# Optimization experiments

Measured on AMD Instinct MI355X. Metric: run time of the kernel, lower is better.

The kernel has to match this reference:

```python
import jax, jax.numpy as jnp
import numpy as np

DILATIONS = [1, 2, 4, 8, 16, 32, 64, 128, 256, 1, 2, 4, 8, 16, 32, 64, 128, 256]
KSIZE = 3
CHAN = 16
NUM_SIG = 1       # num_channels in original
NUM_CTRL = 3      # control channels appended to signal
FRAME_SIZE = 2048
R = sum(d * (KSIZE - 1) for d in DILATIONS) + 1  # 2045
BATCH = 64
T = FRAME_SIZE + R - 1  # 4092


def causal_conv1d(x, w, b, dil):
    # x: [B,T,Cin], w: [K,Cin,Cout] (Keras layout), causal left pad dil*(K-1)
    pad = dil * (w.shape[0] - 1)
    y = jax.lax.conv_general_dilated(
        x, w, window_strides=(1,), padding=[(pad, 0)],
        rhs_dilation=(dil,), dimension_numbers=("NWC", "WIO", "NWC"))
    return y + b


def setup_inputs() -> dict:
    key = jax.random.key(0)
    ks = jax.random.split(key, 8)
    n_layers = len(DILATIONS)
    in0 = NUM_SIG + NUM_CTRL            # layer 0 sees 1 signal + 3 controls = 4
    in_rest = CHAN + NUM_CTRL           # layers 1.. see 16-ch signal + 3 controls = 19
    s = 0.1
    inp = {
        "input": jax.random.normal(ks[0], (BATCH, T, in0), dtype=jnp.float32),
        "conv_w0": jax.random.normal(ks[1], (KSIZE, in0, CHAN), dtype=jnp.float32) * s,
        "conv_w": jax.random.normal(ks[2], (n_layers - 1, KSIZE, in_rest, CHAN), dtype=jnp.float32) * s,
        "conv_b": jax.random.normal(ks[3], (n_layers, CHAN), dtype=jnp.float32) * s,
        "io_w": jax.random.normal(ks[4], (n_layers - 1, CHAN, CHAN), dtype=jnp.float32) * s,
        "io_b": jax.random.normal(ks[5], (n_layers - 1, CHAN), dtype=jnp.float32) * s,
        "mixer_w": jax.random.normal(ks[6], (n_layers * CHAN, NUM_SIG), dtype=jnp.float32) * s,
        "mixer_b": jax.random.normal(ks[7], (NUM_SIG,), dtype=jnp.float32) * s,
    }
    return inp


def reference(input, conv_w0, conv_w, conv_b, io_w, io_b, mixer_w, mixer_b):
    signal = input[:, :, :NUM_SIG]        # [B,T,1]
    controls = input[:, :, NUM_SIG:]      # [B,T,3]
    n_layers = len(DILATIONS)
    acc = []
    for i in range(n_layers):
        w = conv_w0 if i == 0 else conv_w[i - 1]
        h = jnp.concatenate([signal, controls], axis=2)
        h = causal_conv1d(h, w, conv_b[i], DILATIONS[i])
        h = jax.nn.relu(h)                # [B,T,16]
        acc.append(h)
        if i != n_layers - 1:
            # 1x1 conv residual mix + halved channel-sum skip of previous signal
            signal = (jnp.einsum("btc,co->bto", h, io_w[i]) + io_b[i]
                      + jnp.sum(signal, axis=2, keepdims=True) / 2)
    accumulator = jnp.concatenate(acc, axis=2)  # [B,T,288]
    mixed = jnp.einsum("btc,co->bto", accumulator, mixer_w) + mixer_b
    return mixed[:, -FRAME_SIZE:, :]
```

## Files before the change

### kernel.cpp

```cpp
#include <hip/hip_runtime.h>

#define TFULL 4092
#define NB    64
#define CH    16
#define OUT_T 2048
#define TOFF  2044
#define GNT   512

template<int L0, int NL, int TILE, int HALO, bool FIRSTG>
__global__ __launch_bounds__(GNT, 4) void group2_kernel(
    const float* __restrict__ input,
    const float* __restrict__ conv_w0,
    const float* __restrict__ conv_w,
    const float* __restrict__ conv_b,
    const float* __restrict__ io_w,
    const float* __restrict__ io_b,
    const float* __restrict__ mixer_w,
    const float* __restrict__ mixer_b,
    const float* __restrict__ sig_in,
    float* __restrict__ sig_out,
    float* __restrict__ out,
    int out_start)
{
    constexpr int NROWS = TILE + HALO;
    __shared__ float4 buf4[4][NROWS];
    float4* pl0 = buf4[0]; float4* pl1 = buf4[1];
    float4* pl2 = buf4[2]; float4* pl3 = buf4[3];

    const int b       = blockIdx.y;
    const int tid     = threadIdx.x;
    const int tile_lo = out_start + blockIdx.x * TILE;
    const int tile_hi = (tile_lo + TILE < TFULL) ? (tile_lo + TILE) : TFULL;
    const int buf_lo  = tile_lo - HALO;
    const int jmax    = tile_hi - buf_lo;
    const int j0      = NROWS - 1024 + tid;
    const int j1      = NROWS - 512 + tid;

    const float4* ib4 = (const float4*)(input + (size_t)b * TFULL * 4);

    if constexpr (!FIRSTG) {
        const float* sp = sig_in + (size_t)b * TFULL * CH;
        for (int j = tid; j < jmax; j += GNT) {
            const float4* row = (const float4*)(sp + (size_t)(buf_lo + j) * CH);
            pl0[j] = row[0]; pl1[j] = row[1]; pl2[j] = row[2]; pl3[j] = row[3];
        }
        __syncthreads();
    }

    float acc0 = 0.f, acc1 = 0.f;
    int lo_off = 0;
    for (int i = 0; i < NL; ++i) {
        const int g   = L0 + i;
        const int dil = 1 << (g % 9);
        lo_off += 2 * dil;
        const bool lastl = (i == NL - 1);
        const float* wb   = (FIRSTG && g == 0) ? conv_w0
                                               : conv_w + (size_t)(g - 1) * 3 * 19 * CH;
        const float* bias = conv_b  + (size_t)g * CH;
        const float* iw   = io_w    + (size_t)g * CH * CH;
        const float* ob   = io_b    + (size_t)g * CH;
        const float* mw   = mixer_w + (size_t)g * CH;

        const bool a0 = (j0 >= lo_off) && (j0 < jmax);
        const bool a1 = (j1 >= lo_off) && (j1 < jmax);

        float sn0[CH], sn1[CH];

        auto row_compute = [&](int j, float* sn, float& accr) {
            float h[CH];
            #pragma unroll
            for (int o = 0; o < CH; ++o) h[o] = bias[o];
            float sum;
            if (FIRSTG && g == 0) {
                const float4 x0 = ib4[buf_lo + j - 2];
                const float4 x1 = ib4[buf_lo + j - 1];
                const float4 x2 = ib4[buf_lo + j];
                const float t0[4] = {x0.x, x0.y, x0.z, x0.w};
                const float t1[4] = {x1.x, x1.y, x1.z, x1.w};
                const float t2[4] = {x2.x, x2.y, x2.z, x2.w};
                #pragma unroll
                for (int cc = 0; cc < 4; ++cc) {
                    #pragma unroll
                    for (int o = 0; o < CH; ++o) {
                        h[o] = fmaf(t0[cc], wb[(0 * 4 + cc) * CH + o], h[o]);
                        h[o] = fmaf(t1[cc], wb[(1 * 4 + cc) * CH + o], h[o]);
                        h[o] = fmaf(t2[cc], wb[(2 * 4 + cc) * CH + o], h[o]);
                    }
                }
                sum = x2.x;
            } else {
                sum = 0.f;
                #pragma unroll
                for (int k = 0; k < 3; ++k) {
                    const int jm = j - (2 - k) * dil;
                    const float4 s0 = pl0[jm], s1v = pl1[jm],
                                 s2v = pl2[jm], s3v = pl3[jm];
                    const float4 x  = ib4[buf_lo + jm];
                    const float tv[19] = {s0.x, s0.y, s0.z, s0.w,
                                          s1v.x, s1v.y, s1v.z, s1v.w,
                                          s2v.x, s2v.y, s2v.z, s2v.w,
                                          s3v.x, s3v.y, s3v.z, s3v.w,
                                          x.y, x.z, x.w};
                    if (k == 2)
                        sum = ((s0.x + s0.y) + (s0.z + s0.w))
                            + ((s1v.x + s1v.y) + (s1v.z + s1v.w))
                            + ((s2v.x + s2v.y) + (s2v.z + s2v.w))
                            + ((s3v.x + s3v.y) + (s3v.z + s3v.w));
                    #pragma unroll
                    for (int cc = 0; cc < 19; ++cc) {
                        #pragma unroll
                        for (int o = 0; o < CH; ++o)
                            h[o] = fmaf(tv[cc], wb[(k * 19 + cc) * CH + o], h[o]);
                    }
                }
            }
            #pragma unroll
            for (int o = 0; o < CH; ++o) h[o] = fmaxf(h[o], 0.f);

            const int r = buf_lo + j;
            if (j >= HALO && r >= TOFF) {
                float d = 0.f;
                #pragma unroll
                for (int o = 0; o < CH; ++o) d = fmaf(h[o], mw[o], d);
                accr += d;
            }
            const float half = 0.5f * sum;
            #pragma unroll
            for (int o = 0; o < CH; ++o) sn[o] = ob[o] + half;
            #pragma unroll
            for (int cc = 0; cc < CH; ++cc) {
                #pragma unroll
                for (int o = 0; o < CH; ++o)
                    sn[o] = fmaf(h[cc], iw[cc * CH + o], sn[o]);
            }
        };

        if (a0) row_compute(j0, sn0, acc0);
        if (a1) row_compute(j1, sn1, acc1);

        if (!lastl) {
            __syncthreads();
            if (a0) {
                pl0[j0] = make_float4(sn0[0],  sn0[1],  sn0[2],  sn0[3]);
                pl1[j0] = make_float4(sn0[4],  sn0[5],  sn0[6],  sn0[7]);
                pl2[j0] = make_float4(sn0[8],  sn0[9],  sn0[10], sn0[11]);
                pl3[j0] = make_float4(sn0[12], sn0[13], sn0[14], sn0[15]);
            }
            if (a1) {
                pl0[j1] = make_float4(sn1[0],  sn1[1],  sn1[2],  sn1[3]);
                pl1[j1] = make_float4(sn1[4],  sn1[5],  sn1[6],  sn1[7]);
                pl2[j1] = make_float4(sn1[8],  sn1[9],  sn1[10], sn1[11]);
                pl3[j1] = make_float4(sn1[12], sn1[13], sn1[14], sn1[15]);
            }
            __syncthreads();
        } else {
            if (a0) {
                float* gp = sig_out + ((size_t)b * TFULL + (buf_lo + j0)) * CH;
                *(float4*)(gp + 0)  = make_float4(sn0[0],  sn0[1],  sn0[2],  sn0[3]);
                *(float4*)(gp + 4)  = make_float4(sn0[4],  sn0[5],  sn0[6],  sn0[7]);
                *(float4*)(gp + 8)  = make_float4(sn0[8],  sn0[9],  sn0[10], sn0[11]);
                *(float4*)(gp + 12) = make_float4(sn0[12], sn0[13], sn0[14], sn0[15]);
            }
            if (a1) {
                float* gp = sig_out + ((size_t)b * TFULL + (buf_lo + j1)) * CH;
                *(float4*)(gp + 0)  = make_float4(sn1[0],  sn1[1],  sn1[2],  sn1[3]);
                *(float4*)(gp + 4)  = make_float4(sn1[4],  sn1[5],  sn1[6],  sn1[7]);
                *(float4*)(gp + 8)  = make_float4(sn1[8],  sn1[9],  sn1[10], sn1[11]);
                *(float4*)(gp + 12) = make_float4(sn1[12], sn1[13], sn1[14], sn1[15]);
            }
        }
    }

    if (j0 >= HALO && j0 < jmax) {
        const int r = buf_lo + j0;
        if (r >= TOFF) {
            const size_t oi = (size_t)b * OUT_T + (r - TOFF);
            if constexpr (FIRSTG) out[oi] = mixer_b[0] + acc0; else out[oi] += acc0;
        }
    }
    if (j1 >= HALO && j1 < jmax) {
        const int r = buf_lo + j1;
        if (r >= TOFF) {
            const size_t oi = (size_t)b * OUT_T + (r - TOFF);
            if constexpr (FIRSTG) out[oi] = mixer_b[0] + acc1; else out[oi] += acc1;
        }
    }
}

template<bool LASTL>
__global__ __launch_bounds__(256, 4) void single_layer(
    const float* __restrict__ input,
    const float* __restrict__ sig_in,
    const float* __restrict__ w,
    const float* __restrict__ bias,
    const float* __restrict__ iw,
    const float* __restrict__ iob,
    const float* __restrict__ mw,
    float* __restrict__ sig_out,
    float* __restrict__ out,
    int dil, int t0)
{
    const int b = blockIdx.y;
    const int t = t0 + blockIdx.x * 256 + threadIdx.x;
    if (t >= TFULL) return;
    const float* ib = input  + (size_t)b * TFULL * 4;
    const float* sb = sig_in + (size_t)b * TFULL * CH;

    const int tt0 = t - 2 * dil, tt1 = t - dil;
    const float4* sp0 = (const float4*)(sb + (size_t)tt0 * CH);
    const float4* sp1 = (const float4*)(sb + (size_t)tt1 * CH);
    const float4* sp2 = (const float4*)(sb + (size_t)t   * CH);
    const float4 a0 = sp0[0], a1 = sp0[1], a2 = sp0[2], a3 = sp0[3];
    const float4 b0 = sp1[0], b1 = sp1[1], b2 = sp1[2], b3 = sp1[3];
    const float4 c0 = sp2[0], c1 = sp2[1], c2 = sp2[2], c3 = sp2[3];
    const float4 x0 = *(const float4*)(ib + (size_t)tt0 * 4);
    const float4 x1 = *(const float4*)(ib + (size_t)tt1 * 4);
    const float4 x2 = *(const float4*)(ib + (size_t)t   * 4);

    float h[CH];
    #pragma unroll
    for (int o = 0; o < CH; ++o) h[o] = bias[o];

    const float t0v[19] = {a0.x,a0.y,a0.z,a0.w, a1.x,a1.y,a1.z,a1.w,
                           a2.x,a2.y,a2.z,a2.w, a3.x,a3.y,a3.z,a3.w,
                           x0.y,x0.z,x0.w};
    const float t1v[19] = {b0.x,b0.y,b0.z,b0.w, b1.x,b1.y,b1.z,b1.w,
                           b2.x,b2.y,b2.z,b2.w, b3.x,b3.y,b3.z,b3.w,
                           x1.y,x1.z,x1.w};
    const float t2v[19] = {c0.x,c0.y,c0.z,c0.w, c1.x,c1.y,c1.z,c1.w,
                           c2.x,c2.y,c2.z,c2.w, c3.x,c3.y,c3.z,c3.w,
                           x2.y,x2.z,x2.w};
    #pragma unroll
    for (int cc = 0; cc < 19; ++cc) {
        #pragma unroll
        for (int o = 0; o < CH; ++o) {
            h[o] = fmaf(t0v[cc], w[(0 * 19 + cc) * CH + o], h[o]);
            h[o] = fmaf(t1v[cc], w[(1 * 19 + cc) * CH + o], h[o]);
            h[o] = fmaf(t2v[cc], w[(2 * 19 + cc) * CH + o], h[o]);
        }
    }
    #pragma unroll
    for (int o = 0; o < CH; ++o) h[o] = fmaxf(h[o], 0.f);

    if (t >= TOFF) {
        float m = 0.f;
        #pragma unroll
        for (int o = 0; o < CH; ++o) m = fmaf(h[o], mw[o], m);
        out[(size_t)b * OUT_T + (t - TOFF)] += m;
    }

    if constexpr (!LASTL) {
        const float sum_t = ((c0.x + c0.y) + (c0.z + c0.w)) + ((c1.x + c1.y) + (c1.z + c1.w))
                          + ((c2.x + c2.y) + (c2.z + c2.w)) + ((c3.x + c3.y) + (c3.z + c3.w));
        float sn[CH];
        const float half = 0.5f * sum_t;
        #pragma unroll
        for (int o = 0; o < CH; ++o) sn[o] = iob[o] + half;
        #pragma unroll
        for (int cc = 0; cc < CH; ++cc) {
            #pragma unroll
            for (int o = 0; o < CH; ++o)
                sn[o] = fmaf(h[cc], iw[cc * CH + o], sn[o]);
        }
        float* gp = sig_out + ((size_t)b * TFULL + t) * CH;
        *(float4*)(gp + 0)  = make_float4(sn[0],  sn[1],  sn[2],  sn[3]);
        *(float4*)(gp + 4)  = make_float4(sn[4],  sn[5],  sn[6],  sn[7]);
        *(float4*)(gp + 8)  = make_float4(sn[8],  sn[9],  sn[10], sn[11]);
        *(float4*)(gp + 12) = make_float4(sn[12], sn[13], sn[14], sn[15]);
    }
}

extern "C" void kernel_launch(void* const* d_in, const int* in_sizes, int n_in,
                              void* d_out, int out_size, void* d_ws, size_t ws_size,
                              hipStream_t stream) {
    const float* input   = (const float*)d_in[0];
    const float* conv_w0 = (const float*)d_in[1];
    const float* conv_w  = (const float*)d_in[2];
    const float* conv_b  = (const float*)d_in[3];
    const float* io_w    = (const float*)d_in[4];
    const float* io_b    = (const float*)d_in[5];
    const float* mixer_w = (const float*)d_in[6];
    const float* mixer_b = (const float*)d_in[7];
    float* out = (float*)d_out;

    float* s1 = (float*)d_ws;
    float* s2 = s1 + (size_t)NB * TFULL * CH;

    auto wl  = [&](int g) { return conv_w + (size_t)(g - 1) * 3 * 19 * CH; };
    auto bsl = [&](int g) { return conv_b + (size_t)g * CH; };
    auto iwl = [&](int g) { return io_w + (size_t)g * CH * CH; };
    auto ibl = [&](int g) { return io_b + (size_t)g * CH; };
    auto mwl = [&](int g) { return mixer_w + (size_t)g * CH; };

    dim3 blkG(GNT, 1, 1), blk256(256, 1, 1);

    group2_kernel<0, 7, 480, 254, true><<<dim3(8, NB), blkG, 0, stream>>>(
        input, conv_w0, conv_w, conv_b, io_w, io_b, mixer_w, mixer_b,
        nullptr, s1, out, 254);
    single_layer<false><<<dim3(14, NB), blk256, 0, stream>>>(
        input, s1, wl(7), bsl(7), iwl(7), ibl(7), mwl(7), s2, out, 128, 510);
    single_layer<false><<<dim3(12, NB), blk256, 0, stream>>>(
        input, s2, wl(8), bsl(8), iwl(8), ibl(8), mwl(8), s1, out, 256, 1022);
    group2_kernel<9, 8, 320, 510, false><<<dim3(8, NB), blkG, 0, stream>>>(
        input, conv_w0, conv_w, conv_b, io_w, io_b, mixer_w, mixer_b,
        s1, s2, out, 1532);
    single_layer<true><<<dim3(8, NB), blk256, 0, stream>>>(
        input, s2, wl(17), bsl(17), nullptr, nullptr, mwl(17), nullptr, out, 256, 2044);
}
```

Baseline: 306.3 us.

## Stage input controls in LDS, use wave-uniform activity, and re-split layer groups

The grouped kernel now copies the control/input channels into a fifth shared-memory plane, so dilated taps read LDS instead of global memory. Per-thread row activity is replaced by a wave-uniform check built on readfirstlane, which keeps branches non-divergent. The layer loop is kept rolled with unroll 1. The second group now covers layers 9-15 with a smaller halo, and layer 16 runs as its own single_layer launch; single_layer clamps t instead of returning early. The aim is less global traffic and redundant halo compute, paid for with an extra kernel launch and extra LDS per block, which may lower occupancy.

```diff
diff --git a/kernel.cpp b/kernel.cpp
--- a/kernel.cpp
+++ b/kernel.cpp
@@ -7,8 +7,12 @@
 #define TOFF  2044
 #define GNT   512
 
+__device__ __forceinline__ int wave_first(int v) {
+    return __builtin_amdgcn_readfirstlane(v);
+}
+
 template<int L0, int NL, int TILE, int HALO, bool FIRSTG>
-__global__ __launch_bounds__(GNT, 4) void group2_kernel(
+__global__ __launch_bounds__(GNT, 4) void group3_kernel(
     const float* __restrict__ input,
     const float* __restrict__ conv_w0,
     const float* __restrict__ conv_w,
@@ -23,9 +27,7 @@
     int out_start)
 {
     constexpr int NROWS = TILE + HALO;
-    __shared__ float4 buf4[4][NROWS];
-    float4* pl0 = buf4[0]; float4* pl1 = buf4[1];
-    float4* pl2 = buf4[2]; float4* pl3 = buf4[3];
+    __shared__ float4 pl0[NROWS], pl1[NROWS], pl2[NROWS], pl3[NROWS], plx[NROWS];
 
     const int b       = blockIdx.y;
     const int tid     = threadIdx.x;
@@ -34,47 +36,44 @@
     const int buf_lo  = tile_lo - HALO;
     const int jmax    = tile_hi - buf_lo;
     const int j0      = NROWS - 1024 + tid;
-    const int j1      = NROWS - 512 + tid;
+    const int j1      = NROWS - 512  + tid;
 
     const float4* ib4 = (const float4*)(input + (size_t)b * TFULL * 4);
 
-    if constexpr (!FIRSTG) {
-        const float* sp = sig_in + (size_t)b * TFULL * CH;
-        for (int j = tid; j < jmax; j += GNT) {
-            const float4* row = (const float4*)(sp + (size_t)(buf_lo + j) * CH);
+    for (int j = tid; j < jmax; j += GNT) {
+        plx[j] = ib4[buf_lo + j];
+        if constexpr (!FIRSTG) {
+            const float4* row = (const float4*)(sig_in + ((size_t)b * TFULL + buf_lo + j) * CH);
             pl0[j] = row[0]; pl1[j] = row[1]; pl2[j] = row[2]; pl3[j] = row[3];
         }
-        __syncthreads();
-    }
+    }
+    __syncthreads();
 
     float acc0 = 0.f, acc1 = 0.f;
+    float sn0[CH], sn1[CH];
     int lo_off = 0;
+
+    #pragma unroll 1
     for (int i = 0; i < NL; ++i) {
         const int g   = L0 + i;
         const int dil = 1 << (g % 9);
         lo_off += 2 * dil;
-        const bool lastl = (i == NL - 1);
-        const float* wb   = (FIRSTG && g == 0) ? conv_w0
+        const float* wb   = (FIRSTG && i == 0) ? conv_w0
                                                : conv_w + (size_t)(g - 1) * 3 * 19 * CH;
         const float* bias = conv_b  + (size_t)g * CH;
         const float* iw   = io_w    + (size_t)g * CH * CH;
         const float* ob   = io_b    + (size_t)g * CH;
         const float* mw   = mixer_w + (size_t)g * CH;
 
-        const bool a0 = (j0 >= lo_off) && (j0 < jmax);
-        const bool a1 = (j1 >= lo_off) && (j1 < jmax);
-
-        float sn0[CH], sn1[CH];
-
-        auto row_compute = [&](int j, float* sn, float& accr) {
+        auto do_row = [&](int j, float* sn, float& acc) {
             float h[CH];
             #pragma unroll
             for (int o = 0; o < CH; ++o) h[o] = bias[o];
             float sum;
-            if (FIRSTG && g == 0) {
-                const float4 x0 = ib4[buf_lo + j - 2];
-                const float4 x1 = ib4[buf_lo + j - 1];
-                const float4 x2 = ib4[buf_lo + j];
+            if (FIRSTG && i == 0) {
+                const float4 x0 = plx[max(j - 2, 0)];
+                const float4 x1 = plx[max(j - 1, 0)];
+                const float4 x2 = plx[max(j, 0)];
                 const float t0[4] = {x0.x, x0.y, x0.z, x0.w};
                 const float t1[4] = {x1.x, x1.y, x1.z, x1.w};
                 const float t2[4] = {x2.x, x2.y, x2.z, x2.w};
@@ -92,20 +91,15 @@
                 sum = 0.f;
                 #pragma unroll
                 for (int k = 0; k < 3; ++k) {
-                    const int jm = j - (2 - k) * dil;
-                    const float4 s0 = pl0[jm], s1v = pl1[jm],
-                                 s2v = pl2[jm], s3v = pl3[jm];
-                    const float4 x  = ib4[buf_lo + jm];
-                    const float tv[19] = {s0.x, s0.y, s0.z, s0.w,
-                                          s1v.x, s1v.y, s1v.z, s1v.w,
-                                          s2v.x, s2v.y, s2v.z, s2v.w,
-                                          s3v.x, s3v.y, s3v.z, s3v.w,
+                    const int jm = max(j - (2 - k) * dil, 0);
+                    const float4 s0 = pl0[jm], s1 = pl1[jm], s2 = pl2[jm], s3 = pl3[jm];
+                    const float4 x  = plx[jm];
+                    if (k == 2)
+                        sum = ((s0.x + s0.y) + (s0.z + s0.w)) + ((s1.x + s1.y) + (s1.z + s1.w))
+                            + ((s2.x + s2.y) + (s2.z + s2.w)) + ((s3.x + s3.y) + (s3.z + s3.w));
+                    const float tv[19] = {s0.x, s0.y, s0.z, s0.w, s1.x, s1.y, s1.z, s1.w,
+                                          s2.x, s2.y, s2.z, s2.w, s3.x, s3.y, s3.z, s3.w,
                                           x.y, x.z, x.w};
-                    if (k == 2)
-                        sum = ((s0.x + s0.y) + (s0.z + s0.w))
-                            + ((s1v.x + s1v.y) + (s1v.z + s1v.w))
-                            + ((s2v.x + s2v.y) + (s2v.z + s2v.w))
-                            + ((s3v.x + s3v.y) + (s3v.z + s3v.w));
                     #pragma unroll
                     for (int cc = 0; cc < 19; ++cc) {
                         #pragma unroll
@@ -118,11 +112,11 @@
             for (int o = 0; o < CH; ++o) h[o] = fmaxf(h[o], 0.f);
 
             const int r = buf_lo + j;
-            if (j >= HALO && r >= TOFF) {
+            if (j >= HALO && j < jmax && r >= TOFF) {
                 float d = 0.f;
                 #pragma unroll
                 for (int o = 0; o < CH; ++o) d = fmaf(h[o], mw[o], d);
-                accr += d;
+                acc += d;
             }
             const float half = 0.5f * sum;
             #pragma unroll
@@ -135,38 +129,40 @@
             }
         };
 
-        if (a0) row_compute(j0, sn0, acc0);
-        if (a1) row_compute(j1, sn1, acc1);
-
-        if (!lastl) {
+        const bool w1 = (wave_first(j1) + 63 >= lo_off);
+        const bool w0 = (wave_first(j0) + 63 >= lo_off);
+        if (w1) do_row(j1, sn1, acc1);
+        if (w0) do_row(j0, sn0, acc0);
+
+        if (i != NL - 1) {
             __syncthreads();
-            if (a0) {
+            if (w1 && j1 >= lo_off && j1 < jmax) {
+                pl0[j1] = make_float4(sn1[0],  sn1[1],  sn1[2],  sn1[3]);
+                pl1[j1] = make_float4(sn1[4],  sn1[5],  sn1[6],  sn1[7]);
+                pl2[j1] = make_float4(sn1[8],  sn1[9],  sn1[10], sn1[11]);
+                pl3[j1] = make_float4(sn1[12], sn1[13], sn1[14], sn1[15]);
+            }
+            if (w0 && j0 >= lo_off && j0 < jmax) {
                 pl0[j0] = make_float4(sn0[0],  sn0[1],  sn0[2],  sn0[3]);
                 pl1[j0] = make_float4(sn0[4],  sn0[5],  sn0[6],  sn0[7]);
                 pl2[j0] = make_float4(sn0[8],  sn0[9],  sn0[10], sn0[11]);
                 pl3[j0] = make_float4(sn0[12], sn0[13], sn0[14], sn0[15]);
             }
-            if (a1) {
-                pl0[j1] = make_float4(sn1[0],  sn1[1],  sn1[2],  sn1[3]);
-                pl1[j1] = make_float4(sn1[4],  sn1[5],  sn1[6],  sn1[7]);
-                pl2[j1] = make_float4(sn1[8],  sn1[9],  sn1[10], sn1[11]);
-                pl3[j1] = make_float4(sn1[12], sn1[13], sn1[14], sn1[15]);
-            }
             __syncthreads();
         } else {
-            if (a0) {
+            if (j1 >= HALO && j1 < jmax) {
+                float* gp = sig_out + ((size_t)b * TFULL + (buf_lo + j1)) * CH;
+                *(float4*)(gp + 0)  = make_float4(sn1[0],  sn1[1],  sn1[2],  sn1[3]);
+                *(float4*)(gp + 4)  = make_float4(sn1[4],  sn1[5],  sn1[6],  sn1[7]);
+                *(float4*)(gp + 8)  = make_float4(sn1[8],  sn1[9],  sn1[10], sn1[11]);
+                *(float4*)(gp + 12) = make_float4(sn1[12], sn1[13], sn1[14], sn1[15]);
+            }
+            if (j0 >= HALO && j0 < jmax) {
                 float* gp = sig_out + ((size_t)b * TFULL + (buf_lo + j0)) * CH;
                 *(float4*)(gp + 0)  = make_float4(sn0[0],  sn0[1],  sn0[2],  sn0[3]);
                 *(float4*)(gp + 4)  = make_float4(sn0[4],  sn0[5],  sn0[6],  sn0[7]);
                 *(float4*)(gp + 8)  = make_float4(sn0[8],  sn0[9],  sn0[10], sn0[11]);
                 *(float4*)(gp + 12) = make_float4(sn0[12], sn0[13], sn0[14], sn0[15]);
-            }
-            if (a1) {
-                float* gp = sig_out + ((size_t)b * TFULL + (buf_lo + j1)) * CH;
-                *(float4*)(gp + 0)  = make_float4(sn1[0],  sn1[1],  sn1[2],  sn1[3]);
-                *(float4*)(gp + 4)  = make_float4(sn1[4],  sn1[5],  sn1[6],  sn1[7]);
-                *(float4*)(gp + 8)  = make_float4(sn1[8],  sn1[9],  sn1[10], sn1[11]);
-                *(float4*)(gp + 12) = make_float4(sn1[12], sn1[13], sn1[14], sn1[15]);
             }
         }
     }
@@ -200,9 +196,9 @@
     float* __restrict__ out,
     int dil, int t0)
 {
-    const int b = blockIdx.y;
-    const int t = t0 + blockIdx.x * 256 + threadIdx.x;
-    if (t >= TFULL) return;
+    const int b    = blockIdx.y;
+    const int traw = t0 + blockIdx.x * 256 + threadIdx.x;
+    const int t    = (traw < TFULL) ? traw : (TFULL - 1);
     const float* ib = input  + (size_t)b * TFULL * 4;
     const float* sb = sig_in + (size_t)b * TFULL * CH;
 
@@ -242,11 +238,11 @@
     #pragma unroll
     for (int o = 0; o < CH; ++o) h[o] = fmaxf(h[o], 0.f);
 
-    if (t >= TOFF) {
+    if (traw < TFULL && traw >= TOFF) {
         float m = 0.f;
         #pragma unroll
         for (int o = 0; o < CH; ++o) m = fmaf(h[o], mw[o], m);
-        out[(size_t)b * OUT_T + (t - TOFF)] += m;
+        out[(size_t)b * OUT_T + (traw - TOFF)] += m;
     }
 
     if constexpr (!LASTL) {
@@ -262,11 +258,13 @@
             for (int o = 0; o < CH; ++o)
                 sn[o] = fmaf(h[cc], iw[cc * CH + o], sn[o]);
         }
-        float* gp = sig_out + ((size_t)b * TFULL + t) * CH;
-        *(float4*)(gp + 0)  = make_float4(sn[0],  sn[1],  sn[2],  sn[3]);
-        *(float4*)(gp + 4)  = make_float4(sn[4],  sn[5],  sn[6],  sn[7]);
-        *(float4*)(gp + 8)  = make_float4(sn[8],  sn[9],  sn[10], sn[11]);
-        *(float4*)(gp + 12) = make_float4(sn[12], sn[13], sn[14], sn[15]);
+        if (traw < TFULL) {
+            float* gp = sig_out + ((size_t)b * TFULL + traw) * CH;
+            *(float4*)(gp + 0)  = make_float4(sn[0],  sn[1],  sn[2],  sn[3]);
+            *(float4*)(gp + 4)  = make_float4(sn[4],  sn[5],  sn[6],  sn[7]);
+            *(float4*)(gp + 8)  = make_float4(sn[8],  sn[9],  sn[10], sn[11]);
+            *(float4*)(gp + 12) = make_float4(sn[12], sn[13], sn[14], sn[15]);
+        }
     }
 }
 
@@ -294,16 +292,18 @@
 
     dim3 blkG(GNT, 1, 1), blk256(256, 1, 1);
 
-    group2_kernel<0, 7, 480, 254, true><<<dim3(8, NB), blkG, 0, stream>>>(
+    group3_kernel<0, 7, 480, 254, true><<<dim3(8, NB), blkG, 0, stream>>>(
         input, conv_w0, conv_w, conv_b, io_w, io_b, mixer_w, mixer_b,
         nullptr, s1, out, 254);
     single_layer<false><<<dim3(14, NB), blk256, 0, stream>>>(
         input, s1, wl(7), bsl(7), iwl(7), ibl(7), mwl(7), s2, out, 128, 510);
     single_layer<false><<<dim3(12, NB), blk256, 0, stream>>>(
         input, s2, wl(8), bsl(8), iwl(8), ibl(8), mwl(8), s1, out, 256, 1022);
-    group2_kernel<9, 8, 320, 510, false><<<dim3(8, NB), blkG, 0, stream>>>(
+    group3_kernel<9, 7, 352, 254, false><<<dim3(8, NB), blkG, 0, stream>>>(
         input, conv_w0, conv_w, conv_b, io_w, io_b, mixer_w, mixer_b,
-        s1, s2, out, 1532);
+        s1, s2, out, 1276);
+    single_layer<false><<<dim3(10, NB), blk256, 0, stream>>>(
+        input, s2, wl(16), bsl(16), iwl(16), ibl(16), mwl(16), s1, out, 128, 1532);
     single_layer<true><<<dim3(8, NB), blk256, 0, stream>>>(
-        input, s2, wl(17), bsl(17), nullptr, nullptr, mwl(17), nullptr, out, 256, 2044);
+        input, s1, wl(17), bsl(17), nullptr, nullptr, mwl(17), nullptr, out, 256, 2044);
 }
```

Result: faster. 294.9 us (-3.7%).
